# Optimization experiments

Hardware: AMD Instinct MI355X
Metric: run time of the kernel (lower is better)

Reference implementation:

```python
import jax, jax.numpy as jnp
import numpy as np

H = 2048           # lstm_size
T = 8              # per_layer_types
NUM_LAYERS = 24    # sampling steps
LSTM_LAYERS = 2    # lstm_num_layers


def setup_inputs() -> dict:
    key = jax.random.key(0)
    ks = jax.random.split(key, 6)
    sc = 1.0 / np.sqrt(H)
    return {
        "g_emb": jax.random.normal(ks[0], (H,), jnp.float32) * sc,
        "w_emb": jax.random.normal(ks[1], (NUM_LAYERS, T, H), jnp.float32) * sc,
        "w_soft": jax.random.normal(ks[2], (H, T), jnp.float32) * sc,
        "w_ih": jax.random.normal(ks[3], (LSTM_LAYERS, 4 * H, H), jnp.float32) * sc,
        "w_hh": jax.random.normal(ks[4], (LSTM_LAYERS, 4 * H, H), jnp.float32) * sc,
        # uniform noise for Gumbel-max sampling (replaces torch.multinomial)
        "u": jax.random.uniform(ks[5], (NUM_LAYERS, T), jnp.float32, 1e-6, 1.0 - 1e-6),
    }


def _lstm_cell(x, h, c, wih, whh):
    # PyTorch gate order: i, f, g, o ; bias=False
    g = wih @ x + whh @ h                      # (4H,)
    i, f, gg, o = jnp.split(g, 4)
    c2 = jax.nn.sigmoid(f) * c + jax.nn.sigmoid(i) * jnp.tanh(gg)
    h2 = jax.nn.sigmoid(o) * jnp.tanh(c2)
    return h2, c2


def reference(g_emb, w_emb, w_soft, w_ih, w_hh, u):
    gumbel = -jnp.log(-jnp.log(u))             # (NUM_LAYERS, T)
    n_lstm = w_ih.shape[0]
    h_dim = g_emb.shape[0]

    def step(carry, xs):
        x, h, c = carry                        # x:(H,), h/c:(n_lstm,H)
        emb_l, gb = xs                         # (T,H), (T,)
        hs, cs = [], []
        inp = x
        for l in range(n_lstm):                # fixed tiny structural loop
            h2, c2 = _lstm_cell(inp, h[l], c[l], w_ih[l], w_hh[l])
            hs.append(h2); cs.append(c2)
            inp = h2
        logits = inp @ w_soft                  # (T,)
        logp = jax.nn.log_softmax(logits)
        idx = jnp.argmax(logp + gb)            # Gumbel-max ~ multinomial(softmax)
        xent = -logp[idx]                      # CrossEntropyLoss((1,T), (1,))
        nxt = emb_l[idx]                       # next step input embedding
        return (nxt, jnp.stack(hs), jnp.stack(cs)), (idx, xent)

    zeros = jnp.zeros((n_lstm, h_dim), g_emb.dtype)
    init = (g_emb, zeros, zeros)
    _, (ids, xents) = jax.lax.scan(step, init, (w_emb, gumbel))
    sample_log_prob = jnp.mean(xents)
    return ids, sample_log_prob
```

## Files before the change

kernel.cpp:

```cpp
#include <hip/hip_runtime.h>
#include <hip/hip_fp16.h>
#include <math.h>

#define H 2048
#define T 8
#define NSTEP 24
#define NBLK 256
#define NTHR 512
#define NGRP 8
#define GRPSZ (NBLK / NGRP)
#define LOFF ((size_t)4 * H * H)

__device__ __forceinline__ float sigmoidf_(float x) { return 1.0f / (1.0f + expf(-x)); }

__device__ __forceinline__ float dot8(float4 w8, const float4 xa, const float4 xb) {
    const __half2* h = reinterpret_cast<const __half2*>(&w8);
    float2 f0 = __half22float2(h[0]);
    float2 f1 = __half22float2(h[1]);
    float2 f2 = __half22float2(h[2]);
    float2 f3 = __half22float2(h[3]);
    return f0.x * xa.x + f0.y * xa.y + f1.x * xa.z + f1.y * xa.w +
           f2.x * xb.x + f2.y * xb.y + f3.x * xb.z + f3.y * xb.w;
}

__global__ void init_ctrl(int* ctrl) {
    int i = threadIdx.x;
    if (i < 1024) ctrl[i] = 0;
}

__device__ __forceinline__ void grid_barrier(char* wsb, int grp) {
    __syncthreads();
    if (threadIdx.x == 0) {
        int* gen  = (int*)wsb;
        int* root = (int*)(wsb + 256);
        int* gcnt = (int*)(wsb + 512 + 256 * grp);
        int g = __hip_atomic_load(gen, __ATOMIC_RELAXED, __HIP_MEMORY_SCOPE_AGENT);
        int a = __hip_atomic_fetch_add(gcnt, 1, __ATOMIC_RELEASE, __HIP_MEMORY_SCOPE_AGENT);
        if (a == GRPSZ - 1) {
            __hip_atomic_store(gcnt, 0, __ATOMIC_RELAXED, __HIP_MEMORY_SCOPE_AGENT);
            int r = __hip_atomic_fetch_add(root, 1, __ATOMIC_ACQ_REL, __HIP_MEMORY_SCOPE_AGENT);
            if (r == NGRP - 1) {
                __hip_atomic_store(root, 0, __ATOMIC_RELAXED, __HIP_MEMORY_SCOPE_AGENT);
                __hip_atomic_fetch_add(gen, 1, __ATOMIC_RELEASE, __HIP_MEMORY_SCOPE_AGENT);
            }
        }
        int spin = 0;
        while (__hip_atomic_load(gen, __ATOMIC_RELAXED, __HIP_MEMORY_SCOPE_AGENT) == g &&
               spin < (1 << 18)) {
            __builtin_amdgcn_s_sleep(2);
            ++spin;
        }
        (void)__hip_atomic_load(gen, __ATOMIC_ACQUIRE, __HIP_MEMORY_SCOPE_AGENT);
    }
    __syncthreads();
}

__global__ __launch_bounds__(NTHR) void arch_sampler(
    const float* __restrict__ g_emb, const float* __restrict__ w_emb,
    const float* __restrict__ w_soft, const float* __restrict__ w_ih,
    const float* __restrict__ w_hh, const float* __restrict__ u,
    float* __restrict__ out, char* __restrict__ wsb) {
    float* part_g = (float*)(wsb + 4096);
    float* h0b[2] = {(float*)(wsb + (64 << 10)), (float*)(wsb + (64 << 10) + H * 4)};
    float* h1b[2] = {(float*)(wsb + (64 << 10) + 2 * H * 4), (float*)(wsb + (64 << 10) + 3 * H * 4)};
    __half* wih_h = (__half*)(wsb + (128 << 10));
    __half* whh_h = wih_h + 2 * LOFF;

    const int tid = threadIdx.x;
    const int lane = tid & 63;
    const int wv = tid >> 6;
    const int j = blockIdx.x * 8 + wv;
    const int grp = blockIdx.x >> 5;
    const int gtid = blockIdx.x * NTHR + tid;
    const int gstride = NBLK * NTHR;

    {
        const int n8 = (int)(2 * LOFF / 8);
        const float4* s4 = reinterpret_cast<const float4*>(w_ih);
        float4* d4 = reinterpret_cast<float4*>(wih_h);
        for (int i = gtid; i < n8; i += gstride) {
            float4 a = s4[2 * i], b = s4[2 * i + 1];
            union { __half2 h[4]; float4 f; } o;
            o.h[0] = __floats2half2_rn(a.x, a.y);
            o.h[1] = __floats2half2_rn(a.z, a.w);
            o.h[2] = __floats2half2_rn(b.x, b.y);
            o.h[3] = __floats2half2_rn(b.z, b.w);
            d4[i] = o.f;
        }
        s4 = reinterpret_cast<const float4*>(w_hh);
        d4 = reinterpret_cast<float4*>(whh_h);
        for (int i = gtid; i < n8; i += gstride) {
            float4 a = s4[2 * i], b = s4[2 * i + 1];
            union { __half2 h[4]; float4 f; } o;
            o.h[0] = __floats2half2_rn(a.x, a.y);
            o.h[1] = __floats2half2_rn(a.z, a.w);
            o.h[2] = __floats2half2_rn(b.x, b.y);
            o.h[3] = __floats2half2_rn(b.z, b.w);
            d4[i] = o.f;
        }
        for (int i = gtid; i < H; i += gstride) { h0b[0][i] = 0.f; h1b[0][i] = 0.f; }
    }
    grid_barrier(wsb, grp);

    __shared__ float lds_part[8][8];
    __shared__ int s_best;

    const float* xptr = g_emb;
    int pa = 0, pb = 0;
    float c0r = 0.f, c1r = 0.f;
    float xent = 0.f;

    for (int s = 0; s < NSTEP; ++s) {
        {
            const float4* x4 = reinterpret_cast<const float4*>(xptr);
            const float4* h4 = reinterpret_cast<const float4*>(h0b[pa]);
            const float4* wi0 = reinterpret_cast<const float4*>(wih_h + (size_t)(0 * H + j) * H);
            const float4* wi1 = reinterpret_cast<const float4*>(wih_h + (size_t)(1 * H + j) * H);
            const float4* wi2 = reinterpret_cast<const float4*>(wih_h + (size_t)(2 * H + j) * H);
            const float4* wi3 = reinterpret_cast<const float4*>(wih_h + (size_t)(3 * H + j) * H);
            const float4* wh0 = reinterpret_cast<const float4*>(whh_h + (size_t)(0 * H + j) * H);
            const float4* wh1 = reinterpret_cast<const float4*>(whh_h + (size_t)(1 * H + j) * H);
            const float4* wh2 = reinterpret_cast<const float4*>(whh_h + (size_t)(2 * H + j) * H);
            const float4* wh3 = reinterpret_cast<const float4*>(whh_h + (size_t)(3 * H + j) * H);
            float a0 = 0.f, a1 = 0.f, a2 = 0.f, a3 = 0.f;
#pragma unroll
            for (int kk = lane; kk < H / 8; kk += 64) {
                float4 xa = x4[2 * kk], xb = x4[2 * kk + 1];
                float4 ha = h4[2 * kk], hb = h4[2 * kk + 1];
                a0 += dot8(wi0[kk], xa, xb) + dot8(wh0[kk], ha, hb);
                a1 += dot8(wi1[kk], xa, xb) + dot8(wh1[kk], ha, hb);
                a2 += dot8(wi2[kk], xa, xb) + dot8(wh2[kk], ha, hb);
                a3 += dot8(wi3[kk], xa, xb) + dot8(wh3[kk], ha, hb);
            }
#pragma unroll
            for (int off = 1; off < 64; off <<= 1) {
                a0 += __shfl_xor(a0, off, 64);
                a1 += __shfl_xor(a1, off, 64);
                a2 += __shfl_xor(a2, off, 64);
                a3 += __shfl_xor(a3, off, 64);
            }
            float c2 = sigmoidf_(a1) * c0r + sigmoidf_(a0) * tanhf(a2);
            float h2 = sigmoidf_(a3) * tanhf(c2);
            c0r = c2;
            if (lane == 0) h0b[pa ^ 1][j] = h2;
        }
        grid_barrier(wsb, grp);
        pa ^= 1;

        {
            const float4* x4 = reinterpret_cast<const float4*>(h0b[pa]);
            const float4* h4 = reinterpret_cast<const float4*>(h1b[pb]);
            const __half* wiL = wih_h + LOFF;
            const __half* whL = whh_h + LOFF;
            const float4* wi0 = reinterpret_cast<const float4*>(wiL + (size_t)(0 * H + j) * H);
            const float4* wi1 = reinterpret_cast<const float4*>(wiL + (size_t)(1 * H + j) * H);
            const float4* wi2 = reinterpret_cast<const float4*>(wiL + (size_t)(2 * H + j) * H);
            const float4* wi3 = reinterpret_cast<const float4*>(wiL + (size_t)(3 * H + j) * H);
            const float4* wh0 = reinterpret_cast<const float4*>(whL + (size_t)(0 * H + j) * H);
            const float4* wh1 = reinterpret_cast<const float4*>(whL + (size_t)(1 * H + j) * H);
            const float4* wh2 = reinterpret_cast<const float4*>(whL + (size_t)(2 * H + j) * H);
            const float4* wh3 = reinterpret_cast<const float4*>(whL + (size_t)(3 * H + j) * H);
            float a0 = 0.f, a1 = 0.f, a2 = 0.f, a3 = 0.f;
#pragma unroll
            for (int kk = lane; kk < H / 8; kk += 64) {
                float4 xa = x4[2 * kk], xb = x4[2 * kk + 1];
                float4 ha = h4[2 * kk], hb = h4[2 * kk + 1];
                a0 += dot8(wi0[kk], xa, xb) + dot8(wh0[kk], ha, hb);
                a1 += dot8(wi1[kk], xa, xb) + dot8(wh1[kk], ha, hb);
                a2 += dot8(wi2[kk], xa, xb) + dot8(wh2[kk], ha, hb);
                a3 += dot8(wi3[kk], xa, xb) + dot8(wh3[kk], ha, hb);
            }
#pragma unroll
            for (int off = 1; off < 64; off <<= 1) {
                a0 += __shfl_xor(a0, off, 64);
                a1 += __shfl_xor(a1, off, 64);
                a2 += __shfl_xor(a2, off, 64);
                a3 += __shfl_xor(a3, off, 64);
            }
            float c2 = sigmoidf_(a1) * c1r + sigmoidf_(a0) * tanhf(a2);
            float h2 = sigmoidf_(a3) * tanhf(c2);
            c1r = c2;
            if (lane == 0) h1b[pb ^ 1][j] = h2;
            if (lane < 8) lds_part[wv][lane] = h2 * w_soft[(size_t)j * T + lane];
        }
        pb ^= 1;
        __syncthreads();
        if (tid < 8) {
            float p = 0.f;
#pragma unroll
            for (int w = 0; w < 8; ++w) p += lds_part[w][tid];
            part_g[blockIdx.x * 8 + tid] = p;
        }
        grid_barrier(wsb, grp);

        if (wv == 0) {
            const int t = lane & 7;
            const int cch = lane >> 3;
            float acc = 0.f;
            const int b0 = cch * 32;
            for (int b = b0; b < b0 + 32; ++b) acc += part_g[b * 8 + t];
            acc += __shfl_xor(acc, 8, 64);
            acc += __shfl_xor(acc, 16, 64);
            acc += __shfl_xor(acc, 32, 64);
            const float lv = acc;
            float m = lv;
            m = fmaxf(m, __shfl_xor(m, 1, 64));
            m = fmaxf(m, __shfl_xor(m, 2, 64));
            m = fmaxf(m, __shfl_xor(m, 4, 64));
            float se = expf(lv - m);
            se += __shfl_xor(se, 1, 64);
            se += __shfl_xor(se, 2, 64);
            se += __shfl_xor(se, 4, 64);
            const float lse = m + logf(se);
            const float uu = u[s * T + t];
            float v = lv - lse - logf(-logf(uu));
            int bi = t;
#pragma unroll
            for (int off = 1; off < 8; off <<= 1) {
                float ov = __shfl_xor(v, off, 64);
                int oi = __shfl_xor(bi, off, 64);
                if (ov > v || (ov == v && oi < bi)) { v = ov; bi = oi; }
            }
            const float lpb = __shfl(lv, bi, 64) - lse;
            if (tid == 0) {
                xent += -lpb;
                if (blockIdx.x == 0) {
                    out[s] = (float)bi;
                    if (s == NSTEP - 1) out[NSTEP] = xent / (float)NSTEP;
                }
                s_best = bi;
            }
        }
        __syncthreads();
        xptr = w_emb + ((size_t)s * T + s_best) * H;
    }
}

extern "C" void kernel_launch(void* const* d_in, const int* in_sizes, int n_in,
                              void* d_out, int out_size, void* d_ws, size_t ws_size,
                              hipStream_t stream) {
    const float* g_emb  = (const float*)d_in[0];
    const float* w_emb  = (const float*)d_in[1];
    const float* w_soft = (const float*)d_in[2];
    const float* w_ih   = (const float*)d_in[3];
    const float* w_hh   = (const float*)d_in[4];
    const float* u      = (const float*)d_in[5];

    init_ctrl<<<dim3(1), dim3(1024), 0, stream>>>((int*)d_ws);
    arch_sampler<<<dim3(NBLK), dim3(NTHR), 0, stream>>>(
        g_emb, w_emb, w_soft, w_ih, w_hh, u, (float*)d_out, (char*)d_ws);
}
```

Baseline: 1.199 ms.

## Split each LSTM row across two waves with 1024-thread blocks

Block size goes from 512 to 1024 threads, so each hidden row is now computed by two waves that each cover half of the K dimension. Their partial gate sums are combined in LDS, and the cell state moves from registers to shared memory. The intent is more memory-level parallelism per row in the latency-bound GEMV. It also shortens the barrier sleep interval and transposes the logit partial layout so the final reduction reads contiguously. The cost is an extra __syncthreads per layer and a serial epilogue on 8 threads.

New measurement: 1.308 ms. +9.0%, slower.

```diff
diff --git a/kernel.cpp b/kernel.cpp
--- a/kernel.cpp
+++ b/kernel.cpp
@@ -6,7 +6,7 @@
 #define T 8
 #define NSTEP 24
 #define NBLK 256
-#define NTHR 512
+#define NTHR 1024
 #define NGRP 8
 #define GRPSZ (NBLK / NGRP)
 #define LOFF ((size_t)4 * H * H)
@@ -47,7 +47,7 @@
         int spin = 0;
         while (__hip_atomic_load(gen, __ATOMIC_RELAXED, __HIP_MEMORY_SCOPE_AGENT) == g &&
                spin < (1 << 18)) {
-            __builtin_amdgcn_s_sleep(2);
+            __builtin_amdgcn_s_sleep(1);
             ++spin;
         }
         (void)__hip_atomic_load(gen, __ATOMIC_ACQUIRE, __HIP_MEMORY_SCOPE_AGENT);
@@ -69,10 +69,17 @@
     const int tid = threadIdx.x;
     const int lane = tid & 63;
     const int wv = tid >> 6;
-    const int j = blockIdx.x * 8 + wv;
+    const int row = wv >> 1;
+    const int half = wv & 1;
+    const int j = blockIdx.x * 8 + row;
     const int grp = blockIdx.x >> 5;
     const int gtid = blockIdx.x * NTHR + tid;
     const int gstride = NBLK * NTHR;
+
+    __shared__ float part_acc[8][2][4];
+    __shared__ float lds_logit[8][8];
+    __shared__ float c_l[2][8];
+    __shared__ int s_best;
 
     {
         const int n8 = (int)(2 * LOFF / 8);
@@ -99,15 +106,12 @@
             d4[i] = o.f;
         }
         for (int i = gtid; i < H; i += gstride) { h0b[0][i] = 0.f; h1b[0][i] = 0.f; }
+        if (tid < 8) { c_l[0][tid] = 0.f; c_l[1][tid] = 0.f; }
     }
     grid_barrier(wsb, grp);
 
-    __shared__ float lds_part[8][8];
-    __shared__ int s_best;
-
     const float* xptr = g_emb;
     int pa = 0, pb = 0;
-    float c0r = 0.f, c1r = 0.f;
     float xent = 0.f;
 
     for (int s = 0; s < NSTEP; ++s) {
@@ -123,8 +127,9 @@
             const float4* wh2 = reinterpret_cast<const float4*>(whh_h + (size_t)(2 * H + j) * H);
             const float4* wh3 = reinterpret_cast<const float4*>(whh_h + (size_t)(3 * H + j) * H);
             float a0 = 0.f, a1 = 0.f, a2 = 0.f, a3 = 0.f;
-#pragma unroll
-            for (int kk = lane; kk < H / 8; kk += 64) {
+            int kk = half * 128 + lane;
+#pragma unroll
+            for (int it = 0; it < 2; ++it, kk += 64) {
                 float4 xa = x4[2 * kk], xb = x4[2 * kk + 1];
                 float4 ha = h4[2 * kk], hb = h4[2 * kk + 1];
                 a0 += dot8(wi0[kk], xa, xb) + dot8(wh0[kk], ha, hb);
@@ -139,10 +144,23 @@
                 a2 += __shfl_xor(a2, off, 64);
                 a3 += __shfl_xor(a3, off, 64);
             }
-            float c2 = sigmoidf_(a1) * c0r + sigmoidf_(a0) * tanhf(a2);
-            float h2 = sigmoidf_(a3) * tanhf(c2);
-            c0r = c2;
-            if (lane == 0) h0b[pa ^ 1][j] = h2;
+            if (lane == 0) {
+                part_acc[row][half][0] = a0;
+                part_acc[row][half][1] = a1;
+                part_acc[row][half][2] = a2;
+                part_acc[row][half][3] = a3;
+            }
+            __syncthreads();
+            if (tid < 8) {
+                float A0 = part_acc[tid][0][0] + part_acc[tid][1][0];
+                float A1 = part_acc[tid][0][1] + part_acc[tid][1][1];
+                float A2 = part_acc[tid][0][2] + part_acc[tid][1][2];
+                float A3 = part_acc[tid][0][3] + part_acc[tid][1][3];
+                float c2 = sigmoidf_(A1) * c_l[0][tid] + sigmoidf_(A0) * tanhf(A2);
+                float h2 = sigmoidf_(A3) * tanhf(c2);
+                c_l[0][tid] = c2;
+                h0b[pa ^ 1][blockIdx.x * 8 + tid] = h2;
+            }
         }
         grid_barrier(wsb, grp);
         pa ^= 1;
@@ -161,8 +179,9 @@
             const float4* wh2 = reinterpret_cast<const float4*>(whL + (size_t)(2 * H + j) * H);
             const float4* wh3 = reinterpret_cast<const float4*>(whL + (size_t)(3 * H + j) * H);
             float a0 = 0.f, a1 = 0.f, a2 = 0.f, a3 = 0.f;
-#pragma unroll
-            for (int kk = lane; kk < H / 8; kk += 64) {
+            int kk = half * 128 + lane;
+#pragma unroll
+            for (int it = 0; it < 2; ++it, kk += 64) {
                 float4 xa = x4[2 * kk], xb = x4[2 * kk + 1];
                 float4 ha = h4[2 * kk], hb = h4[2 * kk + 1];
                 a0 += dot8(wi0[kk], xa, xb) + dot8(wh0[kk], ha, hb);
@@ -177,28 +196,44 @@
                 a2 += __shfl_xor(a2, off, 64);
                 a3 += __shfl_xor(a3, off, 64);
             }
-            float c2 = sigmoidf_(a1) * c1r + sigmoidf_(a0) * tanhf(a2);
-            float h2 = sigmoidf_(a3) * tanhf(c2);
-            c1r = c2;
-            if (lane == 0) h1b[pb ^ 1][j] = h2;
-            if (lane < 8) lds_part[wv][lane] = h2 * w_soft[(size_t)j * T + lane];
+            if (lane == 0) {
+                part_acc[row][half][0] = a0;
+                part_acc[row][half][1] = a1;
+                part_acc[row][half][2] = a2;
+                part_acc[row][half][3] = a3;
+            }
+            __syncthreads();
+            if (tid < 8) {
+                float A0 = part_acc[tid][0][0] + part_acc[tid][1][0];
+                float A1 = part_acc[tid][0][1] + part_acc[tid][1][1];
+                float A2 = part_acc[tid][0][2] + part_acc[tid][1][2];
+                float A3 = part_acc[tid][0][3] + part_acc[tid][1][3];
+                float c2 = sigmoidf_(A1) * c_l[1][tid] + sigmoidf_(A0) * tanhf(A2);
+                float h2 = sigmoidf_(A3) * tanhf(c2);
+                c_l[1][tid] = c2;
+                h1b[pb ^ 1][blockIdx.x * 8 + tid] = h2;
+                const float* wr = w_soft + (size_t)(blockIdx.x * 8 + tid) * T;
+#pragma unroll
+                for (int t = 0; t < 8; ++t) lds_logit[tid][t] = h2 * wr[t];
+            }
         }
         pb ^= 1;
         __syncthreads();
         if (tid < 8) {
             float p = 0.f;
 #pragma unroll
-            for (int w = 0; w < 8; ++w) p += lds_part[w][tid];
-            part_g[blockIdx.x * 8 + tid] = p;
+            for (int w = 0; w < 8; ++w) p += lds_logit[w][tid];
+            part_g[tid * NBLK + blockIdx.x] = p;
         }
         grid_barrier(wsb, grp);
 
         if (wv == 0) {
             const int t = lane & 7;
             const int cch = lane >> 3;
+            const float* pg = part_g + t * NBLK + cch * 32;
             float acc = 0.f;
-            const int b0 = cch * 32;
-            for (int b = b0; b < b0 + 32; ++b) acc += part_g[b * 8 + t];
+#pragma unroll
+            for (int b = 0; b < 32; ++b) acc += pg[b];
             acc += __shfl_xor(acc, 8, 64);
             acc += __shfl_xor(acc, 16, 64);
             acc += __shfl_xor(acc, 32, 64);
```
